# Optimization experiments

Hardware: AMD Instinct MI355X
Metric: run time of the kernel (lower is better)

## Reference

```python
import jax, jax.numpy as jnp
import numpy as np
import math

DIM = 512


def setup_inputs() -> dict:
    key = jax.random.key(0)
    ks = jax.random.split(key, 6)
    B, N, D = 4, 4096, DIM
    H = D // 2
    features = jax.random.normal(ks[0], (B, N, D), dtype=jnp.float32)
    W1 = jax.random.normal(ks[1], (D, H), dtype=jnp.float32) * 0.02
    b1 = jnp.zeros((H,), dtype=jnp.float32)
    ln_g = jnp.ones((H,), dtype=jnp.float32)
    ln_b = jnp.zeros((H,), dtype=jnp.float32)
    W2 = jax.random.normal(ks[2], (H, 1), dtype=jnp.float32) * 0.02
    b2 = jnp.zeros((1,), dtype=jnp.float32)
    target_entropy = jnp.ones((1,), dtype=jnp.float32) * math.log(D)
    temperature = jnp.ones((1,), dtype=jnp.float32)
    return {"features": features, "W1": W1, "b1": b1, "ln_g": ln_g,
            "ln_b": ln_b, "W2": W2, "b2": b2,
            "target_entropy": target_entropy, "temperature": temperature}


def _layernorm(x, g, b, eps=1e-5):
    mu = jnp.mean(x, axis=-1, keepdims=True)
    var = jnp.mean((x - mu) ** 2, axis=-1, keepdims=True)
    return (x - mu) * jax.lax.rsqrt(var + eps) * g + b


def reference(features, W1, b1, ln_g, ln_b, W2, b2, target_entropy, temperature):
    # ---- compute_entropy: pairwise RBF kernel over [B, N, D] ----
    sq = jnp.sum(features ** 2, axis=-1)                       # [B, N]
    gram = jnp.einsum('bnd,bmd->bnm', features, features)      # [B, N, N]
    d2 = jnp.maximum(sq[:, :, None] + sq[:, None, :] - 2.0 * gram, 0.0)
    tau = temperature[0]
    kernel = jnp.exp(-d2 / (2.0 * tau ** 2))                   # [B, N, N]
    probs = kernel / jnp.sum(kernel, axis=-1, keepdims=True)
    entropy = -jnp.sum(probs * jnp.log(probs + 1e-6), axis=-1)  # [B, N]

    # ---- entropy estimator MLP (computed in original forward, output unused) ----
    h = features @ W1 + b1
    h = _layernorm(h, ln_g, ln_b)
    h = jax.nn.gelu(h, approximate=False)
    estimated_entropy = h @ W2 + b2                            # [B, N, 1] (unused)
    del estimated_entropy

    # ---- sigmoid-gated control signal ----
    entropy_diff = entropy - target_entropy[0]
    control_signal = jax.nn.sigmoid(-entropy_diff / tau)       # [B, N]
    controlled_features = features * control_signal[..., None]
    return controlled_features, control_signal
```

## Files before the change

### kernel.cpp

```cpp
#include <hip/hip_runtime.h>
#include <stdint.h>

#define N_TOK 4096
#define DIM   512
#define BATCH 4
#define BN    (BATCH * N_TOK)
#define JSPLIT 8
#define JT    32
#define IPW   64
#define IPB   256
#define JITERS (N_TOK / JSPLIT / JT)

typedef __attribute__((ext_vector_type(4))) float f32x4;

__global__ __launch_bounds__(256) void prep_kernel(
    const float* __restrict__ feat, uint8_t* __restrict__ fb, float* __restrict__ sq)
{
    int row  = (blockIdx.x << 2) + (threadIdx.x >> 6);
    int lane = threadIdx.x & 63;
    const float4* src = (const float4*)(feat + (size_t)row * DIM);
    float4 v0 = src[lane * 2];
    float4 v1 = src[lane * 2 + 1];

    uint w01 = (uint)__builtin_amdgcn_cvt_pk_fp8_f32(v0.x, v0.y, 0, false);
    w01      = (uint)__builtin_amdgcn_cvt_pk_fp8_f32(v0.z, v0.w, (int)w01, true);
    uint w23 = (uint)__builtin_amdgcn_cvt_pk_fp8_f32(v1.x, v1.y, 0, false);
    w23      = (uint)__builtin_amdgcn_cvt_pk_fp8_f32(v1.z, v1.w, (int)w23, true);
    uint2 pk; pk.x = w01; pk.y = w23;
    ((uint2*)(fb + (size_t)row * DIM))[lane] = pk;

    float s = 0.f, f;
    f = __builtin_amdgcn_cvt_f32_fp8((int)w01, 0); s = fmaf(f, f, s);
    f = __builtin_amdgcn_cvt_f32_fp8((int)w01, 1); s = fmaf(f, f, s);
    f = __builtin_amdgcn_cvt_f32_fp8((int)w01, 2); s = fmaf(f, f, s);
    f = __builtin_amdgcn_cvt_f32_fp8((int)w01, 3); s = fmaf(f, f, s);
    f = __builtin_amdgcn_cvt_f32_fp8((int)w23, 0); s = fmaf(f, f, s);
    f = __builtin_amdgcn_cvt_f32_fp8((int)w23, 1); s = fmaf(f, f, s);
    f = __builtin_amdgcn_cvt_f32_fp8((int)w23, 2); s = fmaf(f, f, s);
    f = __builtin_amdgcn_cvt_f32_fp8((int)w23, 3); s = fmaf(f, f, s);

#pragma unroll
    for (int m = 32; m; m >>= 1) s += __shfl_xor(s, m);
    if (lane == 0) sq[row] = s;
}

__device__ __forceinline__ void dma2(const uint8_t* g, uint8_t* l, int lane, int r)
{
    int loc = lane & 31, h = lane >> 5;
    int sw  = (r + h) & 7;
    const uint8_t* src = g + h * DIM + ((loc ^ sw) << 4);
    __builtin_amdgcn_global_load_lds(
        (const __attribute__((address_space(1))) void*)src,
        (__attribute__((address_space(3))) void*)l, 16, 0, 0);
}

__global__ __launch_bounds__(256, 2) void entropy_kernel(
    const uint8_t* __restrict__ fb, const float* __restrict__ sq,
    const float* __restrict__ temp,
    float* __restrict__ Sp, float* __restrict__ Tp)
{
    __shared__ __align__(16) uint8_t Bs[2][JT * DIM];

    const int t    = threadIdx.x;
    const int w    = t >> 6;
    const int lane = t & 63;
    const int q    = lane >> 4;
    const int c16  = lane & 15;
    const int q1   = q & 1, q2 = q >> 1;
    const int s8   = c16 & 7;

    const int batch  = blockIdx.y;
    const int jh     = blockIdx.z;
    const int iw     = blockIdx.x * IPB + w * IPW;
    const int jstart = jh * (N_TOK / JSPLIT);
    const size_t rowbase = (size_t)batch * N_TOK;

    const float tau    = temp[0];
    const float inv2t2 = 0.5f / (tau * tau);
    const float cg     = 1.0f / (tau * tau);

    long afrag[4][16];
#pragma unroll
    for (int s = 0; s < 4; ++s) {
        const uint2* ap = (const uint2*)(fb + (rowbase + iw + s * 16 + c16) * DIM);
#pragma unroll
        for (int kc = 0; kc < 16; ++kc) {
            uint2 v = ap[kc * 4 + q];
            afrag[s][kc] = (long)(((unsigned long long)v.y << 32) | v.x);
        }
    }
    float pi[4][4];
#pragma unroll
    for (int s = 0; s < 4; ++s)
#pragma unroll
        for (int r = 0; r < 4; ++r)
            pi[s][r] = -sq[rowbase + iw + s * 16 + q * 4 + r] * inv2t2;

    float S[4][4], T[4][4];
#pragma unroll
    for (int s = 0; s < 4; ++s)
#pragma unroll
        for (int r = 0; r < 4; ++r) { S[s][r] = 0.f; T[s][r] = 0.f; }

#pragma unroll
    for (int rr = 0; rr < 4; ++rr) {
        int r = w * 8 + rr * 2;
        dma2(fb + (rowbase + jstart + r) * DIM, &Bs[0][r * DIM], lane, r);
    }
    __syncthreads();

    int cur = 0;
    for (int it = 0; it < JITERS; ++it) {
        const int jb = jstart + it * JT;
        if (it + 1 < JITERS) {
#pragma unroll
            for (int rr = 0; rr < 4; ++rr) {
                int r = w * 8 + rr * 2;
                dma2(fb + (rowbase + jb + JT + r) * DIM, &Bs[cur ^ 1][r * DIM], lane, r);
            }
        }
        float pj0 = -sq[rowbase + jb + c16] * inv2t2;
        float pj1 = -sq[rowbase + jb + 16 + c16] * inv2t2;

#pragma unroll
        for (int jsub = 0; jsub < 2; ++jsub) {
            const uint8_t* Brow = &Bs[cur][(jsub * 16 + c16) * DIM] + (q1 << 3);
            f32x4 acc[4] = {{0,0,0,0},{0,0,0,0},{0,0,0,0},{0,0,0,0}};
#pragma unroll
            for (int kc = 0; kc < 16; ++kc) {
                int off = ((kc * 2 + q2) ^ s8) << 4;
                long b  = *(const long*)(Brow + off);
#pragma unroll
                for (int s = 0; s < 4; ++s)
                    acc[s] = __builtin_amdgcn_mfma_f32_16x16x32_fp8_fp8(
                                 afrag[s][kc], b, acc[s], 0, 0, 0);
            }
            float pj = jsub ? pj1 : pj0;
#pragma unroll
            for (int s = 0; s < 4; ++s)
#pragma unroll
                for (int r = 0; r < 4; ++r) {
                    float e = fminf(fmaf(acc[s][r], cg, pi[s][r] + pj), 0.f);
                    float k = __expf(e);
                    S[s][r] += k;
                    T[s][r] = fmaf(k, e, T[s][r]);
                }
        }
        __syncthreads();
        cur ^= 1;
    }

#pragma unroll
    for (int m = 1; m < 16; m <<= 1)
#pragma unroll
        for (int s = 0; s < 4; ++s)
#pragma unroll
            for (int r = 0; r < 4; ++r) {
                S[s][r] += __shfl_xor(S[s][r], m);
                T[s][r] += __shfl_xor(T[s][r], m);
            }

    if (c16 == 0) {
#pragma unroll
        for (int s = 0; s < 4; ++s)
#pragma unroll
            for (int r = 0; r < 4; ++r) {
                size_t idx = (size_t)jh * BN + rowbase + iw + s * 16 + q * 4 + r;
                Sp[idx] = S[s][r];
                Tp[idx] = T[s][r];
            }
    }
}

__global__ __launch_bounds__(256) void finalize_kernel(
    const float* __restrict__ feat, const float* __restrict__ Sp,
    const float* __restrict__ Tp, const float* __restrict__ tgt,
    const float* __restrict__ temp, float* __restrict__ out)
{
    int row  = (blockIdx.x << 2) + (threadIdx.x >> 6);
    int lane = threadIdx.x & 63;
    float S = 0.0f, T = 0.0f;
#pragma unroll
    for (int j = 0; j < JSPLIT; ++j) {
        S += Sp[(size_t)j * BN + row];
        T += Tp[(size_t)j * BN + row];
    }
    float tau = temp[0];
    float E  = __logf(S) - T / S;
    float cs = 1.0f / (1.0f + __expf((E - tgt[0]) / tau));

    const float4* F4 = (const float4*)(feat + (size_t)row * DIM);
    float4*       O4 = (float4*)(out + (size_t)row * DIM);
    float4 v0 = F4[lane], v1 = F4[lane + 64];
    v0.x *= cs; v0.y *= cs; v0.z *= cs; v0.w *= cs;
    v1.x *= cs; v1.y *= cs; v1.z *= cs; v1.w *= cs;
    O4[lane] = v0; O4[lane + 64] = v1;
    if (lane == 0) out[(size_t)BN * DIM + row] = cs;
}

extern "C" void kernel_launch(void* const* d_in, const int* in_sizes, int n_in,
                              void* d_out, int out_size, void* d_ws, size_t ws_size,
                              hipStream_t stream) {
    const float* feat = (const float*)d_in[0];
    const float* tgt  = (const float*)d_in[7];
    const float* temp = (const float*)d_in[8];
    float* out = (float*)d_out;

    char* ws = (char*)d_ws;
    uint8_t* fb = (uint8_t*)ws;
    float*   sq = (float*)(ws + (size_t)BN * DIM);
    float*   Sp = (float*)(ws + (size_t)BN * DIM + BN * 4);
    float*   Tp = Sp + (size_t)JSPLIT * BN;

    prep_kernel<<<dim3(BN / 4), dim3(256), 0, stream>>>(feat, fb, sq);
    entropy_kernel<<<dim3(N_TOK / IPB, BATCH, JSPLIT), dim3(256), 0, stream>>>(fb, sq, temp, Sp, Tp);
    finalize_kernel<<<dim3(BN / 4), dim3(256), 0, stream>>>(feat, Sp, Tp, tgt, temp, out);
}
```

Measured before the change: 169.7 us.

## Pre-swizzle fp8 features into MFMA fragment layout and skip negligible exp tiles

```diff
diff --git a/kernel.cpp b/kernel.cpp
--- a/kernel.cpp
+++ b/kernel.cpp
@@ -6,73 +6,89 @@
 #define BATCH 4
 #define BN    (BATCH * N_TOK)
 #define JSPLIT 8
-#define JT    32
 #define IPW   64
 #define IPB   256
-#define JITERS (N_TOK / JSPLIT / JT)
+#define NG    (N_TOK / JSPLIT / 16)
 
 typedef __attribute__((ext_vector_type(4))) float f32x4;
 
+__device__ __forceinline__ float sumsq8(uint lo, uint hi) {
+    float s = 0.f, f;
+    f = __builtin_amdgcn_cvt_f32_fp8((int)lo, 0); s = fmaf(f, f, s);
+    f = __builtin_amdgcn_cvt_f32_fp8((int)lo, 1); s = fmaf(f, f, s);
+    f = __builtin_amdgcn_cvt_f32_fp8((int)lo, 2); s = fmaf(f, f, s);
+    f = __builtin_amdgcn_cvt_f32_fp8((int)lo, 3); s = fmaf(f, f, s);
+    f = __builtin_amdgcn_cvt_f32_fp8((int)hi, 0); s = fmaf(f, f, s);
+    f = __builtin_amdgcn_cvt_f32_fp8((int)hi, 1); s = fmaf(f, f, s);
+    f = __builtin_amdgcn_cvt_f32_fp8((int)hi, 2); s = fmaf(f, f, s);
+    f = __builtin_amdgcn_cvt_f32_fp8((int)hi, 3); s = fmaf(f, f, s);
+    return s;
+}
+
 __global__ __launch_bounds__(256) void prep_kernel(
-    const float* __restrict__ feat, uint8_t* __restrict__ fb, float* __restrict__ sq)
+    const float* __restrict__ feat, uint8_t* __restrict__ fb,
+    uint8_t* __restrict__ fbT, float* __restrict__ sq)
 {
-    int row  = (blockIdx.x << 2) + (threadIdx.x >> 6);
-    int lane = threadIdx.x & 63;
-    const float4* src = (const float4*)(feat + (size_t)row * DIM);
-    float4 v0 = src[lane * 2];
-    float4 v1 = src[lane * 2 + 1];
-
-    uint w01 = (uint)__builtin_amdgcn_cvt_pk_fp8_f32(v0.x, v0.y, 0, false);
-    w01      = (uint)__builtin_amdgcn_cvt_pk_fp8_f32(v0.z, v0.w, (int)w01, true);
-    uint w23 = (uint)__builtin_amdgcn_cvt_pk_fp8_f32(v1.x, v1.y, 0, false);
-    w23      = (uint)__builtin_amdgcn_cvt_pk_fp8_f32(v1.z, v1.w, (int)w23, true);
-    uint2 pk; pk.x = w01; pk.y = w23;
-    ((uint2*)(fb + (size_t)row * DIM))[lane] = pk;
-
-    float s = 0.f, f;
-    f = __builtin_amdgcn_cvt_f32_fp8((int)w01, 0); s = fmaf(f, f, s);
-    f = __builtin_amdgcn_cvt_f32_fp8((int)w01, 1); s = fmaf(f, f, s);
-    f = __builtin_amdgcn_cvt_f32_fp8((int)w01, 2); s = fmaf(f, f, s);
-    f = __builtin_amdgcn_cvt_f32_fp8((int)w01, 3); s = fmaf(f, f, s);
-    f = __builtin_amdgcn_cvt_f32_fp8((int)w23, 0); s = fmaf(f, f, s);
-    f = __builtin_amdgcn_cvt_f32_fp8((int)w23, 1); s = fmaf(f, f, s);
-    f = __builtin_amdgcn_cvt_f32_fp8((int)w23, 2); s = fmaf(f, f, s);
-    f = __builtin_amdgcn_cvt_f32_fp8((int)w23, 3); s = fmaf(f, f, s);
-
-#pragma unroll
-    for (int m = 32; m; m >>= 1) s += __shfl_xor(s, m);
-    if (lane == 0) sq[row] = s;
-}
-
-__device__ __forceinline__ void dma2(const uint8_t* g, uint8_t* l, int lane, int r)
-{
-    int loc = lane & 31, h = lane >> 5;
-    int sw  = (r + h) & 7;
-    const uint8_t* src = g + h * DIM + ((loc ^ sw) << 4);
-    __builtin_amdgcn_global_load_lds(
-        (const __attribute__((address_space(1))) void*)src,
-        (__attribute__((address_space(3))) void*)l, 16, 0, 0);
+    __shared__ __align__(8) uint2 lt[1024];
+    const int t = threadIdx.x;
+    const int row16 = t >> 4, seg = t & 15;
+    const size_t grp = blockIdx.x;
+    const size_t row = grp * 16 + row16;
+
+    const float4* src = (const float4*)(feat + row * DIM + seg * 32);
+    uint32_t wd[8];
+    float s = 0.f;
+#pragma unroll
+    for (int i = 0; i < 4; ++i) {
+        float4 a = src[2 * i], b = src[2 * i + 1];
+        uint lo = (uint)__builtin_amdgcn_cvt_pk_fp8_f32(a.x, a.y, 0, false);
+        lo      = (uint)__builtin_amdgcn_cvt_pk_fp8_f32(a.z, a.w, (int)lo, true);
+        uint hi = (uint)__builtin_amdgcn_cvt_pk_fp8_f32(b.x, b.y, 0, false);
+        hi      = (uint)__builtin_amdgcn_cvt_pk_fp8_f32(b.z, b.w, (int)hi, true);
+        wd[2 * i] = lo; wd[2 * i + 1] = hi;
+        s += sumsq8(lo, hi);
+    }
+
+    uint4* dst = (uint4*)(fb + row * DIM + seg * 32);
+    uint4 o0; o0.x = wd[0]; o0.y = wd[1]; o0.z = wd[2]; o0.w = wd[3];
+    uint4 o1; o1.x = wd[4]; o1.y = wd[5]; o1.z = wd[6]; o1.w = wd[7];
+    dst[0] = o0; dst[1] = o1;
+
+#pragma unroll
+    for (int i = 0; i < 4; ++i) {
+        int c = seg * 4 + i;
+        uint2 d; d.x = wd[2 * i]; d.y = wd[2 * i + 1];
+        lt[c * 16 + ((row16 + c) & 15)] = d;
+    }
+
+#pragma unroll
+    for (int m = 1; m < 16; m <<= 1) s += __shfl_xor(s, m);
+    if (seg == 0) sq[row] = s;
+
+    __syncthreads();
+    uint2* ot = (uint2*)(fbT + grp * 8192);
+#pragma unroll
+    for (int i = 0; i < 4; ++i) {
+        int p = t + i * 256;
+        int c = p >> 4, r = p & 15;
+        ot[p] = lt[c * 16 + ((r + c) & 15)];
+    }
 }
 
 __global__ __launch_bounds__(256, 2) void entropy_kernel(
-    const uint8_t* __restrict__ fb, const float* __restrict__ sq,
-    const float* __restrict__ temp,
+    const uint8_t* __restrict__ fb, const uint8_t* __restrict__ fbT,
+    const float* __restrict__ sq, const float* __restrict__ temp,
     float* __restrict__ Sp, float* __restrict__ Tp)
 {
-    __shared__ __align__(16) uint8_t Bs[2][JT * DIM];
-
     const int t    = threadIdx.x;
     const int w    = t >> 6;
     const int lane = t & 63;
     const int q    = lane >> 4;
     const int c16  = lane & 15;
-    const int q1   = q & 1, q2 = q >> 1;
-    const int s8   = c16 & 7;
-
-    const int batch  = blockIdx.y;
-    const int jh     = blockIdx.z;
-    const int iw     = blockIdx.x * IPB + w * IPW;
-    const int jstart = jh * (N_TOK / JSPLIT);
+
+    const int batch = blockIdx.y;
+    const int jh    = blockIdx.z;
+    const int iw    = blockIdx.x * IPB + w * IPW;
     const size_t rowbase = (size_t)batch * N_TOK;
 
     const float tau    = temp[0];
@@ -82,12 +98,9 @@
     long afrag[4][16];
 #pragma unroll
     for (int s = 0; s < 4; ++s) {
-        const uint2* ap = (const uint2*)(fb + (rowbase + iw + s * 16 + c16) * DIM);
-#pragma unroll
-        for (int kc = 0; kc < 16; ++kc) {
-            uint2 v = ap[kc * 4 + q];
-            afrag[s][kc] = (long)(((unsigned long long)v.y << 32) | v.x);
-        }
+        const long* ap = (const long*)(fb + (rowbase + iw + s * 16 + c16) * DIM);
+#pragma unroll
+        for (int kc = 0; kc < 16; ++kc) afrag[s][kc] = ap[kc * 4 + q];
     }
     float pi[4][4];
 #pragma unroll
@@ -102,52 +115,42 @@
 #pragma unroll
         for (int r = 0; r < 4; ++r) { S[s][r] = 0.f; T[s][r] = 0.f; }
 
-#pragma unroll
-    for (int rr = 0; rr < 4; ++rr) {
-        int r = w * 8 + rr * 2;
-        dma2(fb + (rowbase + jstart + r) * DIM, &Bs[0][r * DIM], lane, r);
-    }
-    __syncthreads();
-
-    int cur = 0;
-    for (int it = 0; it < JITERS; ++it) {
-        const int jb = jstart + it * JT;
-        if (it + 1 < JITERS) {
-#pragma unroll
-            for (int rr = 0; rr < 4; ++rr) {
-                int r = w * 8 + rr * 2;
-                dma2(fb + (rowbase + jb + JT + r) * DIM, &Bs[cur ^ 1][r * DIM], lane, r);
+    const long*  bp  = (const long*)fbT
+                     + ((size_t)batch * (N_TOK / 16) + (size_t)jh * NG) * 1024
+                     + q * 16 + c16;
+    const float* sqj = sq + rowbase + jh * (N_TOK / JSPLIT) + c16;
+
+    for (int g = 0; g < NG; ++g) {
+        float pj = -sqj[g * 16] * inv2t2;
+        const long* bg = bp + (size_t)g * 1024;
+        f32x4 acc[4] = {{0,0,0,0},{0,0,0,0},{0,0,0,0},{0,0,0,0}};
+#pragma unroll
+        for (int kc = 0; kc < 16; ++kc) {
+            long b = bg[kc * 64];
+#pragma unroll
+            for (int s = 0; s < 4; ++s)
+                acc[s] = __builtin_amdgcn_mfma_f32_16x16x32_fp8_fp8(
+                             afrag[s][kc], b, acc[s], 0, 0, 0);
+        }
+        float e[4][4], m = -1e30f;
+#pragma unroll
+        for (int s = 0; s < 4; ++s)
+#pragma unroll
+            for (int r = 0; r < 4; ++r) {
+                e[s][r] = fmaf(acc[s][r], cg, pi[s][r] + pj);
+                m = fmaxf(m, e[s][r]);
             }
-        }
-        float pj0 = -sq[rowbase + jb + c16] * inv2t2;
-        float pj1 = -sq[rowbase + jb + 16 + c16] * inv2t2;
-
-#pragma unroll
-        for (int jsub = 0; jsub < 2; ++jsub) {
-            const uint8_t* Brow = &Bs[cur][(jsub * 16 + c16) * DIM] + (q1 << 3);
-            f32x4 acc[4] = {{0,0,0,0},{0,0,0,0},{0,0,0,0},{0,0,0,0}};
-#pragma unroll
-            for (int kc = 0; kc < 16; ++kc) {
-                int off = ((kc * 2 + q2) ^ s8) << 4;
-                long b  = *(const long*)(Brow + off);
-#pragma unroll
-                for (int s = 0; s < 4; ++s)
-                    acc[s] = __builtin_amdgcn_mfma_f32_16x16x32_fp8_fp8(
-                                 afrag[s][kc], b, acc[s], 0, 0, 0);
-            }
-            float pj = jsub ? pj1 : pj0;
+        if (m > -110.0f) {
 #pragma unroll
             for (int s = 0; s < 4; ++s)
 #pragma unroll
                 for (int r = 0; r < 4; ++r) {
-                    float e = fminf(fmaf(acc[s][r], cg, pi[s][r] + pj), 0.f);
-                    float k = __expf(e);
+                    float ee = fminf(e[s][r], 0.f);
+                    float k  = __expf(ee);
                     S[s][r] += k;
-                    T[s][r] = fmaf(k, e, T[s][r]);
+                    T[s][r]  = fmaf(k, ee, T[s][r]);
                 }
         }
-        __syncthreads();
-        cur ^= 1;
     }
 
 #pragma unroll
@@ -207,12 +210,13 @@
     float* out = (float*)d_out;
 
     char* ws = (char*)d_ws;
-    uint8_t* fb = (uint8_t*)ws;
-    float*   sq = (float*)(ws + (size_t)BN * DIM);
-    float*   Sp = (float*)(ws + (size_t)BN * DIM + BN * 4);
-    float*   Tp = Sp + (size_t)JSPLIT * BN;
-
-    prep_kernel<<<dim3(BN / 4), dim3(256), 0, stream>>>(feat, fb, sq);
-    entropy_kernel<<<dim3(N_TOK / IPB, BATCH, JSPLIT), dim3(256), 0, stream>>>(fb, sq, temp, Sp, Tp);
+    uint8_t* fb  = (uint8_t*)ws;
+    uint8_t* fbT = fb + (size_t)BN * DIM;
+    float*   sq  = (float*)(fbT + (size_t)BN * DIM);
+    float*   Sp  = sq + BN;
+    float*   Tp  = Sp + (size_t)JSPLIT * BN;
+
+    prep_kernel<<<dim3(BN / 16), dim3(256), 0, stream>>>(feat, fb, fbT, sq);
+    entropy_kernel<<<dim3(N_TOK / IPB, BATCH, JSPLIT), dim3(256), 0, stream>>>(fb, fbT, sq, temp, Sp, Tp);
     finalize_kernel<<<dim3(BN / 4), dim3(256), 0, stream>>>(feat, Sp, Tp, tgt, temp, out);
 }
```

Result: slower. 173.9 us (+2.5%).
